# Optimization experiments

Measured on AMD Instinct MI355X. Metric: run time of the kernel, lower is better.

Reference implementation:

```python
import jax, jax.numpy as jnp
import numpy as np

B, N, D, DL, DK, DC = 4, 2048, 1024, 64, 128, 8
G_S, G_2, G_1 = 1.0, 0.5, 0.3
EPS = 1e-6

def _christoffel(dk, dl):
    # Poincare-inspired init: for k < min(dk,dl): row/col k set to 0.01, then -0.01 on the diagonal
    G = np.zeros((dk, dl, dl), np.float32)
    idx = np.arange(dl)
    for k in range(min(dk, dl)):
        G[k, k, :] = 0.01
        G[k, :, k] = 0.01
        G[k, idx, idx] -= 0.01
    return jnp.asarray(G)

def setup_inputs() -> dict:
    key = jax.random.key(0)
    ks = jax.random.split(key, 12)
    inp = {
        'x_query': jax.random.normal(ks[0], (B, D), jnp.float32),
        'z_query': 0.1 * jax.random.normal(ks[1], (B, DL), jnp.float32),
        'x_keys': jax.random.normal(ks[2], (B, N, D), jnp.float32),
        'z_keys': 0.1 * jax.random.normal(ks[3], (B, N, DL), jnp.float32),
        'W_Q': jax.random.normal(ks[4], (DK, D), jnp.float32) / np.sqrt(D),
        'W_Qz': jax.random.normal(ks[5], (DK, DL), jnp.float32) / np.sqrt(DL),
        'W_Qgamma': _christoffel(DK, DL),
        'W_K': jax.random.normal(ks[6], (DK, D), jnp.float32) / np.sqrt(D),
        'W_V': jax.random.normal(ks[7], (DK, D), jnp.float32) / np.sqrt(D),
        'W_O': jax.random.normal(ks[8], (D, DK), jnp.float32) / np.sqrt(DK),
        'W_delta': jax.random.normal(ks[9], (DC, DL), jnp.float32) / np.sqrt(DL),
        'basis_b': 0.01 * jax.random.normal(ks[10], (DC, DK, DK), jnp.float32),
        'basis_e': 0.01 * jax.random.normal(ks[11], (DC, DK, DK), jnp.float32),
        'basis_o': 0.01 * jax.random.normal(jax.random.fold_in(key, 99), (DC, DK, DK), jnp.float32),
        'log_sigma': jnp.asarray(np.log(G_S ** 2), jnp.float32),
    }
    return inp

def reference(x_query, z_query, x_keys, z_keys, W_Q, W_Qz, W_Qgamma,
              W_K, W_V, W_O, W_delta, basis_b, basis_e, basis_o, log_sigma):
    dk = W_Q.shape[0]
    # Christoffel query: linear + position + quadratic form  [B, dk]
    q = x_query @ W_Q.T + z_query @ W_Qz.T \
        + jnp.einsum('aij,bi,bj->ba', W_Qgamma, z_query, z_query)
    k = x_keys @ W_K.T            # [B, N, dk]
    v = x_keys @ W_V.T            # [B, N, dk]
    # Wilson line approx: U = I + sum_r coeff_r * (g * skew(basis_r))
    delta = z_query[:, None, :] - z_keys          # [B, N, DL]
    coeff = delta @ W_delta.T                     # [B, N, DC]
    skew = lambda b: b - jnp.swapaxes(b, -1, -2)
    basis = G_S * skew(basis_b) + G_2 * skew(basis_e) + G_1 * skew(basis_o)  # [DC, dk, dk]
    H = jnp.einsum('bnr,rij->bnij', coeff, basis)  # [B, N, dk, dk]
    kt = k + jnp.einsum('bnij,bnj->bni', H, k)     # (I + H) k
    # Conformal temperature tau = sqrt(dk) / lambda(z)
    r_sq = jnp.clip(jnp.sum(z_query ** 2, axis=-1, keepdims=True), None, 1.0 - EPS)
    lam = 2.0 / (1.0 - r_sq + EPS)                 # [B, 1]
    tau = jnp.sqrt(jnp.float32(dk)) / lam
    scores = jnp.einsum('bd,bnd->bn', q, kt) / tau
    attn = jax.nn.softmax(scores, axis=-1)
    # Area-law screening (level=0 -> sigma_eff = sigma)
    dist_sq = jnp.sum(delta ** 2, axis=-1)         # [B, N]
    area = 0.5 * lam ** 2 * dist_sq
    attn = attn * jnp.exp(-jnp.exp(log_sigma) * area)
    out = jnp.einsum('bn,bnd->bd', attn, v) @ W_O.T  # [B, D]
    return out
```

## Files before the change

kernel.cpp:

```cpp
#include <hip/hip_runtime.h>
#include <math.h>


constexpr int XBAR_OFF = 0;
constexpr int CTRL_OFF = 4096;
constexpr int SC_OFF   = 6912;
constexpr int QS_OFF   = 6976;
constexpr int US_OFF   = 7488;
constexpr int AV_OFF   = 11584;
constexpr int WZ_OFF   = 48448;
constexpr int DIST_OFF = 113984;
constexpr int S_OFF    = 122176;
constexpr int WS_FLOATS = 130368;

constexpr int NBLK = 256;
constexpr int MAGIC = 0x1F2E3D4C;
constexpr int CTRL_INTS = 32 * (6 + 5 * 16);

__device__ __forceinline__ float wave_sum(float v) {
#pragma unroll
  for (int off = 32; off > 0; off >>= 1) v += __shfl_xor(v, off, 64);
  return v;
}

__device__ __forceinline__ void pub(float* p, float v) {
  __hip_atomic_store(p, v, __ATOMIC_RELAXED, __HIP_MEMORY_SCOPE_AGENT);
}

__device__ __forceinline__ void gsync(int* ctrl, int phase, int blk) {
  __syncthreads();
  if (threadIdx.x == 0) {
    __builtin_amdgcn_s_waitcnt(0);
    if (phase == 0) {
      while (__hip_atomic_load(ctrl, __ATOMIC_RELAXED,
                               __HIP_MEMORY_SCOPE_AGENT) != MAGIC)
        __builtin_amdgcn_s_sleep(2);
    }
    int* leaf = ctrl + 32 * (6 + phase * 16 + (blk & 15));
    int* root = ctrl + 32 * (1 + phase);
    if (__hip_atomic_fetch_add(leaf, 1, __ATOMIC_RELAXED,
                               __HIP_MEMORY_SCOPE_AGENT) == 15)
      __hip_atomic_fetch_add(root, 1, __ATOMIC_RELAXED,
                             __HIP_MEMORY_SCOPE_AGENT);
    while (__hip_atomic_load(root, __ATOMIC_RELAXED,
                             __HIP_MEMORY_SCOPE_AGENT) < 16)
      __builtin_amdgcn_s_sleep(4);
  }
  __asm__ volatile("" ::: "memory");
  __syncthreads();
}

__global__ __launch_bounds__(256) void k_fused(
    const float* __restrict__ xq, const float* __restrict__ zq,
    const float* __restrict__ x_keys, const float* __restrict__ z_keys,
    const float* __restrict__ WQ, const float* __restrict__ WQz,
    const float* __restrict__ G, const float* __restrict__ WK,
    const float* __restrict__ WV, const float* __restrict__ WO,
    const float* __restrict__ Wd, const float* __restrict__ bb,
    const float* __restrict__ be, const float* __restrict__ bo,
    const float* __restrict__ lsig, float* __restrict__ ws,
    float* __restrict__ out) {
  __shared__ __align__(16) float shm[9824];
  const int tid = threadIdx.x;
  const int blk = blockIdx.x;
  int* ctrl = (int*)(ws + CTRL_OFF);

  if (blk == 0) {
    for (int i = tid; i < CTRL_INTS; i += 256)
      __hip_atomic_store(ctrl + i, 0, __ATOMIC_RELAXED,
                         __HIP_MEMORY_SCOPE_AGENT);
    __syncthreads();
    if (tid == 0)
      __hip_atomic_store(ctrl, MAGIC, __ATOMIC_RELAXED,
                         __HIP_MEMORY_SCOPE_AGENT);
  }

  if (blk < 32) {
    float* xqs = shm;
    float* zqs = shm + 1024;
    float* part = shm + 1088;
    const int b = blk >> 3, as_ = blk & 7;
    for (int i = tid; i < 1024; i += 256) xqs[i] = xq[b * 1024 + i];
    if (tid < 64) zqs[tid] = zq[b * 64 + tid];
    __syncthreads();
    const int seg = tid & 15;
    const int a = as_ * 16 + (tid >> 4);
    const float4* wq4 = (const float4*)(WQ + a * 1024 + seg * 64);
    const float4* xs4 = (const float4*)(xqs + seg * 64);
    float p = 0;
#pragma unroll
    for (int c = 0; c < 16; ++c) {
      float4 w = wq4[c], x = xs4[c];
      p += w.x * x.x + w.y * x.y + w.z * x.z + w.w * x.w;
    }
#pragma unroll
    for (int c = 0; c < 4; ++c)
      p += WQz[a * 64 + seg * 4 + c] * zqs[seg * 4 + c];
#pragma unroll
    for (int ii = 0; ii < 4; ++ii) {
      const int i = seg * 4 + ii;
      const float4* g4 = (const float4*)(G + a * 4096 + i * 64);
      float inner = 0;
#pragma unroll
      for (int c = 0; c < 16; ++c) {
        float4 gv = g4[c];
        const float4 zv = *(const float4*)(zqs + c * 4);
        inner += gv.x * zv.x + gv.y * zv.y + gv.z * zv.z + gv.w * zv.w;
      }
      p += zqs[i] * inner;
    }
    part[tid] = p;
    __syncthreads();
    if (tid < 16) {
      float s = 0;
#pragma unroll
      for (int h = 0; h < 16; ++h) s += part[tid * 16 + h];
      pub(&ws[QS_OFF + b * 128 + as_ * 16 + tid], s);
    }
  } else if (blk < 64) {
    float* sWd = shm;
    float* zqs = shm + 512;
    sWd[tid] = Wd[tid];
    sWd[256 + tid] = Wd[256 + tid];
    zqs[tid] = zq[tid];
    __syncthreads();
    const int bn = (blk - 32) * 256 + tid;
    const int b = bn >> 11;
    const float4* zk4 = (const float4*)(z_keys + (size_t)bn * 64);
    const float* zqb = zqs + b * 64;
    float wzv[8] = {0, 0, 0, 0, 0, 0, 0, 0};
    float dist = 0;
    for (int l4 = 0; l4 < 16; ++l4) {
      float4 z4 = zk4[l4];
      float ze[4] = {z4.x, z4.y, z4.z, z4.w};
#pragma unroll
      for (int e = 0; e < 4; ++e) {
        const int l = l4 * 4 + e;
        float z = ze[e];
        float dz = zqb[l] - z;
        dist += dz * dz;
#pragma unroll
        for (int r = 0; r < 8; ++r) wzv[r] += sWd[r * 64 + l] * z;
      }
    }
#pragma unroll
    for (int r = 0; r < 8; ++r) pub(&ws[WZ_OFF + bn * 8 + r], wzv[r]);
    pub(&ws[DIST_OFF + bn], dist);
  } else if (blk == 64) {
    float* zqs = shm;
    zqs[tid] = zq[tid];
    __syncthreads();
    const int b = tid >> 6, l = tid & 63;
    float z = zqs[b * 64 + l];
    float r2 = wave_sum(z * z);
    float cz[8];
#pragma unroll
    for (int r = 0; r < 8; ++r) cz[r] = wave_sum(Wd[r * 64 + l] * z);
    if (l == 0) {
      r2 = fminf(r2, 1.0f - 1e-6f);
      float lam = 2.0f / (1.0f - r2 + 1e-6f);
      pub(&ws[SC_OFF + b * 16 + 0], lam / sqrtf(128.0f));
      pub(&ws[SC_OFF + b * 16 + 1], expf(lsig[0]) * 0.5f * lam * lam);
#pragma unroll
      for (int r = 0; r < 8; ++r) pub(&ws[SC_OFF + b * 16 + 2 + r], cz[r]);
    }
  } else if (blk < 69) {
    const int b = blk - 65;
    for (int i = tid; i < 1024; i += 256)
      pub(&ws[XBAR_OFF + b * 1024 + i], 0.0f);
  }
  gsync(ctrl, 0, blk);

  if (blk < 64) {
    const int r = blk >> 3, jc = blk & 7;
    float* sq = shm;
    float* red = shm + 512;
    for (int o = tid; o < 512; o += 256) sq[o] = ws[QS_OFF + o];
    __syncthreads();
    const int jl = tid & 15, is = tid >> 4;
    const int j = jc * 16 + jl;
    float acc[4] = {0, 0, 0, 0};
    const float* arrs[3] = {bb, be, bo};
    const float wgt[3] = {1.0f, 0.5f, 0.3f};
#pragma unroll
    for (int arr = 0; arr < 3; ++arr) {
      const float w = wgt[arr];
      const float* base = arrs[arr] + r * 16384;
#pragma unroll
      for (int k = 0; k < 8; ++k) {
        const int i = is * 8 + k;
        const float sk = w * (base[i * 128 + j] - base[j * 128 + i]);
#pragma unroll
        for (int b = 0; b < 4; ++b) acc[b] += sk * sq[b * 128 + i];
      }
    }
#pragma unroll
    for (int b = 0; b < 4; ++b) red[(jl * 4 + b) * 16 + is] = acc[b];
    __syncthreads();
    if (tid < 64) {
      const int jl2 = tid >> 2, b = tid & 3;
      float s = 0;
#pragma unroll
      for (int is2 = 0; is2 < 16; ++is2) s += red[(jl2 * 4 + b) * 16 + is2];
      pub(&ws[US_OFF + b * 1024 + r * 128 + jc * 16 + jl2], s);
    }
  }
  gsync(ctrl, 1, blk);

  if (blk < 64) {
    const int b = blk >> 4, dbase = (blk & 15) * 64;
    float* qu = shm;
    float* part = shm + 1152;
    float* fin = shm + 3456;
    float* czq = shm + 4032;
    for (int o = tid; o < 1152; o += 256)
      qu[o] = (o < 128) ? ws[QS_OFF + b * 128 + o]
                        : ws[US_OFF + b * 1024 + (o - 128)];
    if (tid < 8) czq[tid] = ws[SC_OFF + b * 16 + 2 + tid];
    __syncthreads();
    const int kq = tid >> 6, dloc = tid & 63;
    float acc[9];
#pragma unroll
    for (int jj = 0; jj < 9; ++jj) acc[jj] = 0;
    const float* wkp = WK + dbase + dloc;
#pragma unroll 4
    for (int k = kq * 32; k < kq * 32 + 32; ++k) {
      const float wk = wkp[k * 1024];
#pragma unroll
      for (int jj = 0; jj < 9; ++jj) acc[jj] += qu[jj * 128 + k] * wk;
    }
#pragma unroll
    for (int jj = 0; jj < 9; ++jj) part[kq * 576 + jj * 64 + dloc] = acc[jj];
    __syncthreads();
    for (int o = tid; o < 576; o += 256)
      fin[o] = part[o] + part[576 + o] + part[1152 + o] + part[1728 + o];
    __syncthreads();
    float* av = ws + AV_OFF + b * 9216;
    for (int o = tid; o < 576; o += 256) {
      const int jj = o >> 6, dl = o & 63;
      float val = fin[o];
      if (jj == 0) {
#pragma unroll
        for (int rr = 0; rr < 8; ++rr)
          val += czq[rr] * fin[(1 + rr) * 64 + dl];
      }
      pub(&av[jj * 1024 + dbase + dl], val);
    }
  }
  gsync(ctrl, 2, blk);

  {
    float* sav = shm;
    const int b = blk >> 6;
    const float* avg = ws + AV_OFF + b * 9216;
    for (int i = tid * 4; i < 9216; i += 1024)
      *(float4*)(sav + i) = *(const float4*)(avg + i);
    if (tid == 0) shm[9216] = ws[SC_OFF + b * 16];
    __syncthreads();

    const int wave = tid >> 6, lane = tid & 63;
    for (int half = 0; half < 2; ++half) {
      const int nbase = (blk & 63) * 32 + half * 16 + wave * 4;
      const float* xb = x_keys + ((size_t)(b * 2048 + nbase)) * 1024;

      float acc[9][4];
#pragma unroll
      for (int j = 0; j < 9; ++j)
#pragma unroll
        for (int p = 0; p < 4; ++p) acc[j][p] = 0;

#pragma unroll
      for (int c = 0; c < 4; ++c) {
        const int off = c * 256 + lane * 4;
        float4 xv[4];
#pragma unroll
        for (int p = 0; p < 4; ++p)
          xv[p] = *(const float4*)(xb + p * 1024 + off);
#pragma unroll
        for (int j = 0; j < 9; ++j) {
          float4 a = *(const float4*)(sav + j * 1024 + off);
#pragma unroll
          for (int p = 0; p < 4; ++p)
            acc[j][p] +=
                a.x * xv[p].x + a.y * xv[p].y + a.z * xv[p].z + a.w * xv[p].w;
        }
      }
#pragma unroll
      for (int j = 0; j < 9; ++j)
#pragma unroll
        for (int p = 0; p < 4; ++p) acc[j][p] = wave_sum(acc[j][p]);

      if (lane == 0) {
        const float it = shm[9216];
        for (int p = 0; p < 4; ++p) {
          const int bn = b * 2048 + nbase + p;
          const float* wz = ws + WZ_OFF + bn * 8;
          float s = acc[0][p];
#pragma unroll
          for (int r = 0; r < 8; ++r) s -= wz[r] * acc[1 + r][p];
          pub(&ws[S_OFF + bn], s * it);
        }
      }
    }
  }
  gsync(ctrl, 3, blk);

  {
    const int b = blk >> 6, loc = blk & 63, nt = loc >> 2, dsl = loc & 3;
    float* red = shm;
    float* sw = shm + 256;
    float sv[8];
    float vmax = -1e30f;
#pragma unroll
    for (int i = 0; i < 8; ++i) {
      sv[i] = ws[S_OFF + b * 2048 + i * 256 + tid];
      vmax = fmaxf(vmax, sv[i]);
    }
    red[tid] = vmax;
    __syncthreads();
    for (int s = 128; s > 0; s >>= 1) {
      if (tid < s) red[tid] = fmaxf(red[tid], red[tid + s]);
      __syncthreads();
    }
    const float m = red[0];
    __syncthreads();
    float lsum = 0;
#pragma unroll
    for (int i = 0; i < 8; ++i) lsum += expf(sv[i] - m);
    red[tid] = lsum;
    __syncthreads();
    for (int s = 128; s > 0; s >>= 1) {
      if (tid < s) red[tid] += red[tid + s];
      __syncthreads();
    }
    const float rl = 1.0f / red[0];
    const float screen = ws[SC_OFF + b * 16 + 1];
    const int n0 = nt * 128;
    if (tid < 128) {
      const int n = n0 + tid;
      sw[tid] = expf(ws[S_OFF + b * 2048 + n] - m -
                     screen * ws[DIST_OFF + b * 2048 + n]) * rl;
    }
    __syncthreads();
    const int d = dsl * 256 + tid;
    const float* xb = x_keys + ((size_t)(b * 2048 + n0)) * 1024 + d;
    float a0 = 0, a1 = 0, a2 = 0, a3 = 0;
    for (int n = 0; n < 128; n += 4) {
      a0 += sw[n + 0] * xb[(size_t)(n + 0) * 1024];
      a1 += sw[n + 1] * xb[(size_t)(n + 1) * 1024];
      a2 += sw[n + 2] * xb[(size_t)(n + 2) * 1024];
      a3 += sw[n + 3] * xb[(size_t)(n + 3) * 1024];
    }
    atomicAdd(&ws[XBAR_OFF + b * 1024 + d], (a0 + a1) + (a2 + a3));
  }
  gsync(ctrl, 4, blk);

  if (blk < 16) {
    const int b = blk >> 2, dsl = blk & 3;
    float* sx = shm;
    float* sy = shm + 1024;
    for (int i = tid; i < 1024; i += 256) sx[i] = ws[XBAR_OFF + b * 1024 + i];
    __syncthreads();
    const int wave = tid >> 6, lane = tid & 63;
    for (int t = 0; t < 32; ++t) {
      const int dk = wave * 32 + t;
      const float4* wv4 = (const float4*)(WV + dk * 1024 + lane * 16);
      const float4* xs4 = (const float4*)(sx + lane * 16);
      float p = 0;
#pragma unroll
      for (int c = 0; c < 4; ++c) {
        float4 w4 = wv4[c], x4 = xs4[c];
        p += w4.x * x4.x + w4.y * x4.y + w4.z * x4.z + w4.w * x4.w;
      }
      p = wave_sum(p);
      if (lane == 0) sy[dk] = p;
    }
    __syncthreads();
    const int d = dsl * 256 + tid;
    const float4* wo4 = (const float4*)(WO + d * 128);
    float acc = 0;
#pragma unroll
    for (int c = 0; c < 32; ++c) {
      float4 w = wo4[c];
      acc += w.x * sy[c * 4 + 0] + w.y * sy[c * 4 + 1] +
             w.z * sy[c * 4 + 2] + w.w * sy[c * 4 + 3];
    }
    out[b * 1024 + d] = acc;
  }
}

extern "C" void kernel_launch(void* const* d_in, const int* in_sizes, int n_in,
                              void* d_out, int out_size, void* d_ws,
                              size_t ws_size, hipStream_t stream) {
  const float* xq  = (const float*)d_in[0];
  const float* zq  = (const float*)d_in[1];
  const float* xk  = (const float*)d_in[2];
  const float* zk  = (const float*)d_in[3];
  const float* WQ  = (const float*)d_in[4];
  const float* WQz = (const float*)d_in[5];
  const float* G   = (const float*)d_in[6];
  const float* WK  = (const float*)d_in[7];
  const float* WV  = (const float*)d_in[8];
  const float* WO  = (const float*)d_in[9];
  const float* Wd  = (const float*)d_in[10];
  const float* bb  = (const float*)d_in[11];
  const float* be  = (const float*)d_in[12];
  const float* bo  = (const float*)d_in[13];
  const float* ls  = (const float*)d_in[14];
  float* ws  = (float*)d_ws;
  float* out = (float*)d_out;
  if (ws_size < (size_t)WS_FLOATS * sizeof(float)) return;

  hipLaunchKernelGGL(k_fused, dim3(NBLK), dim3(256), 0, stream,
                     xq, zq, xk, zk, WQ, WQz, G, WK, WV, WO, Wd, bb, be, bo,
                     ls, ws, out);
}
```

Baseline: 174.7 us.

## Replace global barriers with per-stage counters and split final reductions across all blocks

Swaps the tree-style grid barriers for per-stage dataflow counters, so each stage waits only on the producers it actually depends on. The AV stage moves to blocks 64-127, which lets it overlap with other early work. The x_keys weighted sum is rewritten to use float4 loads over 32-key tiles and write deterministic partials instead of atomics, followed by a separate partial-reduction stage. The W_V and W_O projections are spread over all 256 blocks instead of 16. This adds two more global sync stages and a large partial buffer in workspace.

Measured after the change: 176.2 us. About the same (+0.8%).

```diff
diff --git a/kernel.cpp b/kernel.cpp
--- a/kernel.cpp
+++ b/kernel.cpp
@@ -4,18 +4,30 @@
 
 constexpr int XBAR_OFF = 0;
 constexpr int CTRL_OFF = 4096;
-constexpr int SC_OFF   = 6912;
-constexpr int QS_OFF   = 6976;
-constexpr int US_OFF   = 7488;
-constexpr int AV_OFF   = 11584;
-constexpr int WZ_OFF   = 48448;
-constexpr int DIST_OFF = 113984;
-constexpr int S_OFF    = 122176;
-constexpr int WS_FLOATS = 130368;
+constexpr int SC_OFF   = 4608;
+constexpr int QS_OFF   = 4672;
+constexpr int US_OFF   = 5184;
+constexpr int AV_OFF   = 9280;
+constexpr int WZ_OFF   = 46144;
+constexpr int DIST_OFF = 111680;
+constexpr int S_OFF    = 119872;
+constexpr int Y_OFF    = 128064;
+constexpr int PART_OFF = 128576;
+constexpr int WS_FLOATS = 390720;
 
 constexpr int NBLK = 256;
 constexpr int MAGIC = 0x1F2E3D4C;
-constexpr int CTRL_INTS = 32 * (6 + 5 * 16);
+constexpr int C_MAGIC = 0;
+constexpr int C_Q  = 32 * 1;
+constexpr int C_WZ = 32 * 2;
+constexpr int C_SC = 32 * 3;
+constexpr int C_U  = 32 * 4;
+constexpr int C_AV = 32 * 5;
+constexpr int C_S3 = 32 * 6;
+constexpr int C_P4 = 32 * 7;
+constexpr int C_P5 = 32 * 8;
+constexpr int C_Y  = 32 * 9;
+constexpr int CTRL_INTS = 32 * 10;
 
 __device__ __forceinline__ float wave_sum(float v) {
 #pragma unroll
@@ -26,27 +38,23 @@
 __device__ __forceinline__ void pub(float* p, float v) {
   __hip_atomic_store(p, v, __ATOMIC_RELAXED, __HIP_MEMORY_SCOPE_AGENT);
 }
-
-__device__ __forceinline__ void gsync(int* ctrl, int phase, int blk) {
+__device__ __forceinline__ void pub2(float* p, float a, float b) {
+  union { float f[2]; unsigned long long u; } v;
+  v.f[0] = a; v.f[1] = b;
+  __hip_atomic_store((unsigned long long*)p, v.u, __ATOMIC_RELAXED,
+                     __HIP_MEMORY_SCOPE_AGENT);
+}
+
+__device__ __forceinline__ void sig(int* c) {
   __syncthreads();
-  if (threadIdx.x == 0) {
-    __builtin_amdgcn_s_waitcnt(0);
-    if (phase == 0) {
-      while (__hip_atomic_load(ctrl, __ATOMIC_RELAXED,
-                               __HIP_MEMORY_SCOPE_AGENT) != MAGIC)
-        __builtin_amdgcn_s_sleep(2);
-    }
-    int* leaf = ctrl + 32 * (6 + phase * 16 + (blk & 15));
-    int* root = ctrl + 32 * (1 + phase);
-    if (__hip_atomic_fetch_add(leaf, 1, __ATOMIC_RELAXED,
-                               __HIP_MEMORY_SCOPE_AGENT) == 15)
-      __hip_atomic_fetch_add(root, 1, __ATOMIC_RELAXED,
-                             __HIP_MEMORY_SCOPE_AGENT);
-    while (__hip_atomic_load(root, __ATOMIC_RELAXED,
-                             __HIP_MEMORY_SCOPE_AGENT) < 16)
-      __builtin_amdgcn_s_sleep(4);
-  }
-  __asm__ volatile("" ::: "memory");
+  if (threadIdx.x == 0)
+    __hip_atomic_fetch_add(c, 1, __ATOMIC_RELAXED, __HIP_MEMORY_SCOPE_AGENT);
+}
+__device__ __forceinline__ void wait_ge(int* c, int t) {
+  if (threadIdx.x == 0)
+    while (__hip_atomic_load(c, __ATOMIC_RELAXED,
+                             __HIP_MEMORY_SCOPE_AGENT) < t)
+      __builtin_amdgcn_s_sleep(1);
   __syncthreads();
 }
 
@@ -67,13 +75,18 @@
 
   if (blk == 0) {
     for (int i = tid; i < CTRL_INTS; i += 256)
-      __hip_atomic_store(ctrl + i, 0, __ATOMIC_RELAXED,
+      __hip_atomic_store(ctrl + i, (i == C_MAGIC) ? 0 : 0, __ATOMIC_RELAXED,
                          __HIP_MEMORY_SCOPE_AGENT);
     __syncthreads();
     if (tid == 0)
-      __hip_atomic_store(ctrl, MAGIC, __ATOMIC_RELAXED,
+      __hip_atomic_store(ctrl + C_MAGIC, MAGIC, __ATOMIC_RELAXED,
                          __HIP_MEMORY_SCOPE_AGENT);
   }
+  if (tid == 0)
+    while (__hip_atomic_load(ctrl + C_MAGIC, __ATOMIC_RELAXED,
+                             __HIP_MEMORY_SCOPE_AGENT) != MAGIC)
+      __builtin_amdgcn_s_sleep(1);
+  __syncthreads();
 
   if (blk < 32) {
     float* xqs = shm;
@@ -117,6 +130,7 @@
       for (int h = 0; h < 16; ++h) s += part[tid * 16 + h];
       pub(&ws[QS_OFF + b * 128 + as_ * 16 + tid], s);
     }
+    sig(ctrl + C_Q);
   } else if (blk < 64) {
     float* sWd = shm;
     float* zqs = shm + 512;
@@ -146,6 +160,7 @@
 #pragma unroll
     for (int r = 0; r < 8; ++r) pub(&ws[WZ_OFF + bn * 8 + r], wzv[r]);
     pub(&ws[DIST_OFF + bn], dist);
+    sig(ctrl + C_WZ);
   } else if (blk == 64) {
     float* zqs = shm;
     zqs[tid] = zq[tid];
@@ -164,14 +179,11 @@
 #pragma unroll
       for (int r = 0; r < 8; ++r) pub(&ws[SC_OFF + b * 16 + 2 + r], cz[r]);
     }
-  } else if (blk < 69) {
-    const int b = blk - 65;
-    for (int i = tid; i < 1024; i += 256)
-      pub(&ws[XBAR_OFF + b * 1024 + i], 0.0f);
-  }
-  gsync(ctrl, 0, blk);
+    sig(ctrl + C_SC);
+  }
 
   if (blk < 64) {
+    wait_ge(ctrl + C_Q, 32);
     const int r = blk >> 3, jc = blk & 7;
     float* sq = shm;
     float* red = shm + 512;
@@ -204,11 +216,14 @@
       for (int is2 = 0; is2 < 16; ++is2) s += red[(jl2 * 4 + b) * 16 + is2];
       pub(&ws[US_OFF + b * 1024 + r * 128 + jc * 16 + jl2], s);
     }
-  }
-  gsync(ctrl, 1, blk);
-
-  if (blk < 64) {
-    const int b = blk >> 4, dbase = (blk & 15) * 64;
+    sig(ctrl + C_U);
+  }
+
+  if (blk >= 64 && blk < 128) {
+    wait_ge(ctrl + C_U, 64);
+    wait_ge(ctrl + C_SC, 1);
+    const int lb = blk - 64;
+    const int b = lb >> 4, dbase = (lb & 15) * 64;
     float* qu = shm;
     float* part = shm + 1152;
     float* fin = shm + 3456;
@@ -246,10 +261,13 @@
       }
       pub(&av[jj * 1024 + dbase + dl], val);
     }
-  }
-  gsync(ctrl, 2, blk);
+    sig(ctrl + C_AV);
+  }
 
   {
+    wait_ge(ctrl + C_AV, 64);
+    wait_ge(ctrl + C_WZ, 32);
+    wait_ge(ctrl + C_SC, 1);
     float* sav = shm;
     const int b = blk >> 6;
     const float* avg = ws + AV_OFF + b * 9216;
@@ -302,11 +320,12 @@
         }
       }
     }
-  }
-  gsync(ctrl, 3, blk);
+    sig(ctrl + C_S3);
+  }
 
   {
-    const int b = blk >> 6, loc = blk & 63, nt = loc >> 2, dsl = loc & 3;
+    wait_ge(ctrl + C_S3, 256);
+    const int b = blk >> 6, nt = blk & 63, n0 = nt * 32;
     float* red = shm;
     float* sw = shm + 256;
     float sv[8];
@@ -335,57 +354,93 @@
     }
     const float rl = 1.0f / red[0];
     const float screen = ws[SC_OFF + b * 16 + 1];
-    const int n0 = nt * 128;
-    if (tid < 128) {
+    if (tid < 32) {
       const int n = n0 + tid;
       sw[tid] = expf(ws[S_OFF + b * 2048 + n] - m -
                      screen * ws[DIST_OFF + b * 2048 + n]) * rl;
     }
     __syncthreads();
-    const int d = dsl * 256 + tid;
-    const float* xb = x_keys + ((size_t)(b * 2048 + n0)) * 1024 + d;
-    float a0 = 0, a1 = 0, a2 = 0, a3 = 0;
-    for (int n = 0; n < 128; n += 4) {
-      a0 += sw[n + 0] * xb[(size_t)(n + 0) * 1024];
-      a1 += sw[n + 1] * xb[(size_t)(n + 1) * 1024];
-      a2 += sw[n + 2] * xb[(size_t)(n + 2) * 1024];
-      a3 += sw[n + 3] * xb[(size_t)(n + 3) * 1024];
-    }
-    atomicAdd(&ws[XBAR_OFF + b * 1024 + d], (a0 + a1) + (a2 + a3));
-  }
-  gsync(ctrl, 4, blk);
-
-  if (blk < 16) {
-    const int b = blk >> 2, dsl = blk & 3;
-    float* sx = shm;
-    float* sy = shm + 1024;
-    for (int i = tid; i < 1024; i += 256) sx[i] = ws[XBAR_OFF + b * 1024 + i];
-    __syncthreads();
-    const int wave = tid >> 6, lane = tid & 63;
-    for (int t = 0; t < 32; ++t) {
-      const int dk = wave * 32 + t;
-      const float4* wv4 = (const float4*)(WV + dk * 1024 + lane * 16);
-      const float4* xs4 = (const float4*)(sx + lane * 16);
-      float p = 0;
-#pragma unroll
-      for (int c = 0; c < 4; ++c) {
-        float4 w4 = wv4[c], x4 = xs4[c];
-        p += w4.x * x4.x + w4.y * x4.y + w4.z * x4.z + w4.w * x4.w;
-      }
+    const float4* xb4 =
+        (const float4*)(x_keys + ((size_t)(b * 2048 + n0)) * 1024);
+    float4 acc = {0, 0, 0, 0};
+#pragma unroll 4
+    for (int n = 0; n < 32; ++n) {
+      const float w = sw[n];
+      float4 x = xb4[n * 256 + tid];
+      acc.x += w * x.x; acc.y += w * x.y;
+      acc.z += w * x.z; acc.w += w * x.w;
+    }
+    float* pw = ws + PART_OFF + ((b * 64 + nt) << 10) + tid * 4;
+    pub2(pw, acc.x, acc.y);
+    pub2(pw + 2, acc.z, acc.w);
+    sig(ctrl + C_P4);
+  }
+
+  {
+    wait_ge(ctrl + C_P4, 256);
+    const int b = blk >> 6, d0 = (blk & 63) * 16;
+    const int nt = tid >> 2, q = tid & 3;
+    float4 v = *(const float4*)(ws + PART_OFF + ((b * 64 + nt) << 10) + d0 +
+                                q * 4);
+    float4* shm4 = (float4*)shm;
+    shm4[tid] = v;
+    __syncthreads();
+    for (int s = 32; s > 0; s >>= 1) {
+      if (nt < s) {
+        float4 a = shm4[tid], c = shm4[tid + s * 4];
+        a.x += c.x; a.y += c.y; a.z += c.z; a.w += c.w;
+        shm4[tid] = a;
+      }
+      __syncthreads();
+    }
+    if (tid < 4) {
+      float4 a = shm4[tid];
+      float* p = ws + XBAR_OFF + b * 1024 + d0 + tid * 4;
+      pub2(p, a.x, a.y);
+      pub2(p + 2, a.z, a.w);
+    }
+    sig(ctrl + C_P5);
+  }
+
+  {
+    wait_ge(ctrl + C_P5, 256);
+    for (int t = blk; t < 512; t += 256) {
+      const int b = t >> 7, dk = t & 127;
+      const float4* wv4 = (const float4*)(WV + dk * 1024);
+      const float4* xb4 = (const float4*)(ws + XBAR_OFF + b * 1024);
+      float4 w = wv4[tid], x = xb4[tid];
+      float p = w.x * x.x + w.y * x.y + w.z * x.z + w.w * x.w;
       p = wave_sum(p);
-      if (lane == 0) sy[dk] = p;
-    }
-    __syncthreads();
-    const int d = dsl * 256 + tid;
-    const float4* wo4 = (const float4*)(WO + d * 128);
-    float acc = 0;
-#pragma unroll
-    for (int c = 0; c < 32; ++c) {
-      float4 w = wo4[c];
-      acc += w.x * sy[c * 4 + 0] + w.y * sy[c * 4 + 1] +
-             w.z * sy[c * 4 + 2] + w.w * sy[c * 4 + 3];
-    }
-    out[b * 1024 + d] = acc;
+      if ((tid & 63) == 0) shm[tid >> 6] = p;
+      __syncthreads();
+      if (tid == 0)
+        pub(&ws[Y_OFF + b * 128 + dk], shm[0] + shm[1] + shm[2] + shm[3]);
+      __syncthreads();
+    }
+    sig(ctrl + C_Y);
+  }
+
+  {
+    wait_ge(ctrl + C_Y, 256);
+    const int b = blk >> 6, d0 = (blk & 63) * 16;
+    float* sy = shm;
+    float* part = shm + 128;
+    if (tid < 128) sy[tid] = ws[Y_OFF + b * 128 + tid];
+    __syncthreads();
+    const int dloc = tid >> 4, seg = tid & 15;
+    const float4* wo4 = (const float4*)(WO + (d0 + dloc) * 128 + seg * 8);
+    const float4* sy4 = (const float4*)(sy + seg * 8);
+    float4 w0 = wo4[0], w1 = wo4[1], y0 = sy4[0], y1 = sy4[1];
+    float p = w0.x * y0.x + w0.y * y0.y + w0.z * y0.z + w0.w * y0.w +
+              w1.x * y1.x + w1.y * y1.y + w1.z * y1.z + w1.w * y1.w;
+    part[tid] = p;
+    __syncthreads();
+    if (tid < 16) {
+      float s = 0;
+#pragma unroll
+      for (int h = 0; h < 16; ++h) s += part[tid * 16 + h];
+      out[b * 1024 + d0 + tid] = s;
+    }
   }
 }
 
```
